# Optimization experiments

Measured on AMD Instinct MI355X. Metric: run time of the kernel, lower is better.

## Reference

```python
import jax, jax.numpy as jnp
import numpy as np

SCALE = 0.0078125  # dequant scale from init_kwargs


def setup_inputs() -> dict:
    key = jax.random.key(0)
    k1, k2, k3 = jax.random.split(key, 3)
    B, S, D_IN, D_OUT = 4, 2048, 2048, 8192
    x = jax.random.normal(k1, (B, S, D_IN), dtype=jnp.float32)
    weight = jax.random.normal(k2, (D_OUT, D_IN), dtype=jnp.float32)  # torch Linear layout
    bias = jax.random.normal(k3, (D_OUT,), dtype=jnp.float32)
    return {"x": x, "weight": weight, "bias": bias}


def reference(x, weight, bias):
    # MATMUL.apply(x, weight.t(), bias, scale): scaled matmul + fused bias
    # out[b,s,o] = scale * sum_i x[b,s,i] * weight[o,i] + bias[o]
    out = jnp.einsum('bsi,oi->bso', x, weight) * jnp.asarray(SCALE, x.dtype)
    return out + bias
```

## Files before the change

kernel.cpp:

```cpp
#include <hip/hip_runtime.h>
#include <hip/hip_bf16.h>
#include <stdint.h>

typedef __bf16 bf16x8 __attribute__((ext_vector_type(8)));
typedef float  f32x4  __attribute__((ext_vector_type(4)));
typedef float  f32x16 __attribute__((ext_vector_type(16)));

static constexpr float kScale = 0.0078125f;

static __device__ __forceinline__ uint32_t bf16_rne(float f) {
  uint32_t u = __builtin_bit_cast(uint32_t, f);
  u += 0x7FFFu + ((u >> 16) & 1u);
  return u >> 16;
}
static __device__ __forceinline__ uint32_t pack2(float lo, float hi) {
  return bf16_rne(lo) | (bf16_rne(hi) << 16);
}

__global__ __launch_bounds__(256) void cvt_fused(
    const float* __restrict__ x, const float* __restrict__ w,
    uint4* __restrict__ dst, long nx8 ) {
  const long i = (long)blockIdx.x * 256 + threadIdx.x;
  const float4* sv;
  long j;
  if (i < nx8) { sv = reinterpret_cast<const float4*>(x); j = i; }
  else         { sv = reinterpret_cast<const float4*>(w); j = i - nx8; }
  float4 a = sv[2 * j];
  float4 b = sv[2 * j + 1];
  uint4 o;
  o.x = pack2(a.x, a.y);
  o.y = pack2(a.z, a.w);
  o.z = pack2(b.x, b.y);
  o.w = pack2(b.z, b.w);
  dst[i] = o;
}

__global__ __launch_bounds__(256) void cvt_f32_to_bf16(
    const float* __restrict__ src, uint4* __restrict__ dst) {
  const int i = blockIdx.x * 256 + threadIdx.x;
  const float4* sv = reinterpret_cast<const float4*>(src);
  float4 a = sv[2 * i];
  float4 b = sv[2 * i + 1];
  uint4 o;
  o.x = pack2(a.x, a.y);
  o.y = pack2(a.z, a.w);
  o.z = pack2(b.x, b.y);
  o.w = pack2(b.z, b.w);
  dst[i] = o;
}

static __device__ __forceinline__ void gload_lds16(const void* g, void* l) {
  __builtin_amdgcn_global_load_lds(
      (const __attribute__((address_space(1))) void*)g,
      (__attribute__((address_space(3))) void*)l, 16, 0, 0);
}

#define BARRIER() __builtin_amdgcn_s_barrier()
#define VMW(n) asm volatile("s_waitcnt vmcnt(" #n ")" ::: "memory")

constexpr int TILE_V = (256 * 64) / 8;

template <int MH, int NH>
__device__ __forceinline__ void quad32(f32x16 (&acc)[4][2],
                                       const bf16x8 (&aF)[2][4],
                                       const bf16x8 (&bF)[4]) {
  __builtin_amdgcn_s_setprio(1);
#pragma unroll
  for (int ks = 0; ks < 4; ++ks)
#pragma unroll
    for (int mt = 0; mt < 2; ++mt)
      acc[MH * 2 + mt][NH] = __builtin_amdgcn_mfma_f32_32x32x16_bf16(
          aF[mt][ks], bF[ks], acc[MH * 2 + mt][NH], 0, 0, 0);
  __builtin_amdgcn_s_setprio(0);
}

template <int BUF, int MH>
__device__ __forceinline__ void loadA32(bf16x8 (&aF)[2][4], const bf16x8* Av,
                                        int wr, int l31, int erk) {
#pragma unroll
  for (int ks = 0; ks < 4; ++ks)
#pragma unroll
    for (int mt = 0; mt < 2; ++mt) {
      const int row = (MH << 7) + (wr << 6) + (mt << 5) + l31;
      aF[mt][ks] = Av[BUF * TILE_V + row * 8 + ((ks << 1) ^ erk)];
    }
}
template <int BUF, int NH>
__device__ __forceinline__ void loadB32(bf16x8 (&bF)[4], const bf16x8* Bv,
                                        int wc, int l31, int erk) {
  const int row = (NH << 7) + (wc << 5) + l31;
#pragma unroll
  for (int ks = 0; ks < 4; ++ks)
    bF[ks] = Bv[BUF * TILE_V + row * 8 + ((ks << 1) ^ erk)];
}

__global__ __launch_bounds__(512, 2) void gemm256_8phase(
    const uint16_t* __restrict__ A, const uint16_t* __restrict__ B,
    const float* __restrict__ bias, float* __restrict__ C,
    int Mi, int Ni, int Ki) {
  __shared__ __align__(16) uint16_t As[2][256 * 64];
  __shared__ __align__(16) uint16_t Bs[2][256 * 64];

  const int tid = threadIdx.x;
  const int l   = tid & 63;
  const int wv  = tid >> 6;
  const int wr  = wv >> 2;
  const int wc  = wv & 3;
  const int l31 = l & 31;
  const int lk  = l >> 5;
  const int l8  = l >> 3;
  const int l7  = l & 7;

  const int erk = l7 ^ ((l31 >> 3) & 3) ^ lk ^ (lk << 2);

  const int nbm = Mi >> 8, nbn = Ni >> 8;
  const int nwg = nbm * nbn;
  const int q = nwg >> 3, r = nwg & 7;
  const int xcd = (int)blockIdx.x & 7, orig = (int)blockIdx.x >> 3;
  const int swz = (xcd < r ? xcd * (q + 1) : r * (q + 1) + (xcd - r) * q) + orig;

  int bm, bn;
  if ((nbm & 7) == 0 && (nbn & 3) == 0) {
    const int s = swz >> 5;
    const int o = swz & 31;
    const int nsc = nbn >> 2;
    bm = (s / nsc) * 8 + (o >> 2);
    bn = (s % nsc) * 4 + (o & 3);
  } else {
    bm = swz / nbn;
    bn = swz % nbn;
  }

  const int u0   = l7 ^ l8 ^ (wv & 3);
  const int xcol = (u0 ^ ((u0 & 1) << 2)) << 3;
  const uint16_t* gA0 = A + (size_t)((bm << 8) + (wv << 3) + l8) * Ki + xcol;
  const uint16_t* gB0 = B + (size_t)((bn << 8) + (wv << 3) + l8) * Ki + xcol;

#define STAGE_A(bufi, chunk, t)                        \
  gload_lds16(gA0 + (size_t)(chunk) * Ki + (t) * 64,   \
              &As[bufi][((chunk) + (wv << 3)) << 6])
#define STAGE_B(bufi, chunk, t)                        \
  gload_lds16(gB0 + (size_t)(chunk) * Ki + (t) * 64,   \
              &Bs[bufi][((chunk) + (wv << 3)) << 6])

  const bf16x8* Av = reinterpret_cast<const bf16x8*>(&As[0][0]);
  const bf16x8* Bv = reinterpret_cast<const bf16x8*>(&Bs[0][0]);

  f32x16 acc[4][2] = {};
  bf16x8 aF[2][4], b0[4], b1[4];

  const int NT = Ki >> 6;
  const int NI = NT >> 1;

  STAGE_A(0, 0, 0);   STAGE_A(0, 64, 0);
  STAGE_B(0, 0, 0);   STAGE_B(0, 64, 0);
  STAGE_B(0, 128, 0); STAGE_B(0, 192, 0);
  STAGE_A(0, 128, 0); STAGE_A(0, 192, 0);
  STAGE_A(1, 0, 1);   STAGE_A(1, 64, 1);
  STAGE_B(1, 0, 1);   STAGE_B(1, 64, 1);
  STAGE_B(1, 128, 1); STAGE_B(1, 192, 1);
  VMW(6);
  BARRIER();

#pragma unroll 1
  for (int i = 0; i < NI - 1; ++i) {
    const int t1 = 2 * i + 1, t2 = 2 * i + 2, t3 = 2 * i + 3;

    loadB32<0, 0>(b0, Bv, wc, l31, erk);
    loadA32<0, 0>(aF, Av, wr, l31, erk);
    STAGE_A(1, 128, t1); STAGE_A(1, 192, t1);
    quad32<0, 0>(acc, aF, b0);
    BARRIER();

    loadB32<0, 1>(b1, Bv, wc, l31, erk);
    STAGE_A(0, 0, t2); STAGE_A(0, 64, t2);
    quad32<0, 1>(acc, aF, b1);
    BARRIER();

    loadA32<0, 1>(aF, Av, wr, l31, erk);
    STAGE_B(0, 0, t2); STAGE_B(0, 64, t2);
    quad32<1, 0>(acc, aF, b0);
    BARRIER();

    STAGE_B(0, 128, t2); STAGE_B(0, 192, t2);
    quad32<1, 1>(acc, aF, b1);
    VMW(6);
    BARRIER();

    loadB32<1, 0>(b0, Bv, wc, l31, erk);
    loadA32<1, 0>(aF, Av, wr, l31, erk);
    STAGE_A(0, 128, t2); STAGE_A(0, 192, t2);
    quad32<0, 0>(acc, aF, b0);
    BARRIER();

    loadB32<1, 1>(b1, Bv, wc, l31, erk);
    STAGE_A(1, 0, t3); STAGE_A(1, 64, t3);
    quad32<0, 1>(acc, aF, b1);
    BARRIER();

    loadA32<1, 1>(aF, Av, wr, l31, erk);
    STAGE_B(1, 0, t3); STAGE_B(1, 64, t3);
    quad32<1, 0>(acc, aF, b0);
    BARRIER();

    STAGE_B(1, 128, t3); STAGE_B(1, 192, t3);
    quad32<1, 1>(acc, aF, b1);
    VMW(6);
    BARRIER();
  }

  {
    const int t1 = NT - 1;
    loadB32<0, 0>(b0, Bv, wc, l31, erk);
    loadA32<0, 0>(aF, Av, wr, l31, erk);
    STAGE_A(1, 128, t1); STAGE_A(1, 192, t1);
    quad32<0, 0>(acc, aF, b0);
    BARRIER();
    loadB32<0, 1>(b1, Bv, wc, l31, erk);
    quad32<0, 1>(acc, aF, b1);
    BARRIER();
    loadA32<0, 1>(aF, Av, wr, l31, erk);
    quad32<1, 0>(acc, aF, b0);
    BARRIER();
    quad32<1, 1>(acc, aF, b1);
    VMW(0);
    BARRIER();
    loadB32<1, 0>(b0, Bv, wc, l31, erk);
    loadA32<1, 0>(aF, Av, wr, l31, erk);
    quad32<0, 0>(acc, aF, b0);
    BARRIER();
    loadB32<1, 1>(b1, Bv, wc, l31, erk);
    quad32<0, 1>(acc, aF, b1);
    BARRIER();
    loadA32<1, 1>(aF, Av, wr, l31, erk);
    quad32<1, 0>(acc, aF, b0);
    BARRIER();
    quad32<1, 1>(acc, aF, b1);
  }

  const int rowB = (bm << 8) + (wr << 6) + 4 * lk;
  const int colB = (bn << 8) + (wc << 5) + l31;
#pragma unroll
  for (int mt4 = 0; mt4 < 4; ++mt4) {
    const int rBase = rowB + (mt4 >> 1) * 128 + (mt4 & 1) * 32;
#pragma unroll
    for (int nh = 0; nh < 2; ++nh) {
      const int col = colB + nh * 128;
      const float bv = bias[col];
#pragma unroll
      for (int reg = 0; reg < 16; ++reg) {
        const int row = rBase + (reg & 3) + 8 * (reg >> 2);
        C[(size_t)row * Ni + col] = acc[mt4][nh][reg] * kScale + bv;
      }
    }
  }
}

__global__ __launch_bounds__(256) void gemm_bf16_bias(
    const uint16_t* __restrict__ A, const uint16_t* __restrict__ B,
    const float* __restrict__ bias, float* __restrict__ C,
    int Mi, int Ni, int Ki) {
  __shared__ __align__(16) uint16_t As[128 * 32];
  __shared__ __align__(16) uint16_t Bs[128 * 32];

  const int tid  = threadIdx.x;
  const int lane = tid & 63;
  const int wv   = tid >> 6;
  const int wr   = wv >> 1;
  const int wc   = wv & 1;
  const int fr   = lane & 15;
  const int fh   = lane >> 4;

  const int nTilesN = Ni >> 7;
  const int nwg = gridDim.x;
  const int q = nwg >> 3, r = nwg & 7;
  const int xcd = (int)blockIdx.x & 7, orig = (int)blockIdx.x >> 3;
  const int swz = (xcd < r ? xcd * (q + 1) : r * (q + 1) + (xcd - r) * q) + orig;
  const int bm = swz / nTilesN;
  const int bn = swz % nTilesN;

  const int sRow = tid >> 2;
  const int sCol = (tid & 3) << 3;

  const uint16_t* gA0 = A + (size_t)(bm * 128 + sRow) * Ki + sCol;
  const uint16_t* gA1 = gA0 + (size_t)64 * Ki;
  const uint16_t* gB0 = B + (size_t)(bn * 128 + sRow) * Ki + sCol;
  const uint16_t* gB1 = gB0 + (size_t)64 * Ki;
  uint16_t* lA0 = &As[tid * 8];
  uint16_t* lA1 = &As[(256 + tid) * 8];
  uint16_t* lB0 = &Bs[tid * 8];
  uint16_t* lB1 = &Bs[(256 + tid) * 8];

  const bf16x8* Av = reinterpret_cast<const bf16x8*>(As);
  const bf16x8* Bv = reinterpret_cast<const bf16x8*>(Bs);

  f32x4 acc[4][4] = {};

  for (int k0 = 0; k0 < Ki; k0 += 32) {
    gload_lds16(gA0 + k0, lA0);
    gload_lds16(gA1 + k0, lA1);
    gload_lds16(gB0 + k0, lB0);
    gload_lds16(gB1 + k0, lB1);
    __syncthreads();

    bf16x8 af[4], bfr[4];
#pragma unroll
    for (int m = 0; m < 4; ++m) af[m] = Av[(wr * 64 + m * 16 + fr) * 4 + fh];
#pragma unroll
    for (int n = 0; n < 4; ++n) bfr[n] = Bv[(wc * 64 + n * 16 + fr) * 4 + fh];

#pragma unroll
    for (int m = 0; m < 4; ++m)
#pragma unroll
      for (int n = 0; n < 4; ++n)
        acc[m][n] = __builtin_amdgcn_mfma_f32_16x16x32_bf16(af[m], bfr[n],
                                                            acc[m][n], 0, 0, 0);
    __syncthreads();
  }

  const int rowBase = bm * 128 + wr * 64;
  const int colBase = bn * 128 + wc * 64;
#pragma unroll
  for (int n = 0; n < 4; ++n) {
    const int col = colBase + n * 16 + fr;
    const float bv = bias[col];
#pragma unroll
    for (int m = 0; m < 4; ++m) {
      const int row = rowBase + m * 16 + fh * 4;
#pragma unroll
      for (int j = 0; j < 4; ++j)
        C[(size_t)(row + j) * Ni + col] = acc[m][n][j] * kScale + bv;
    }
  }
}

__global__ void naive_gemm(const float* __restrict__ x, const float* __restrict__ w,
                           const float* __restrict__ bias, float* __restrict__ out,
                           int Mi, int Ni, int Ki) {
  long idx = (long)blockIdx.x * blockDim.x + threadIdx.x;
  if (idx >= (long)Mi * Ni) return;
  int m = (int)(idx / Ni), n = (int)(idx % Ni);
  float s = 0.f;
  for (int k = 0; k < Ki; ++k) s += x[(long)m * Ki + k] * w[(long)n * Ki + k];
  out[idx] = s * kScale + bias[n];
}

extern "C" void kernel_launch(void* const* d_in, const int* in_sizes, int n_in,
                              void* d_out, int out_size, void* d_ws, size_t ws_size,
                              hipStream_t stream) {
  const float* x    = (const float*)d_in[0];
  const float* w    = (const float*)d_in[1];
  const float* bias = (const float*)d_in[2];
  float* out = (float*)d_out;

  const int Ni = in_sizes[2];
  const int Ki = in_sizes[1] / Ni;
  const int Mi = in_sizes[0] / Ki;

  const size_t nx = (size_t)Mi * Ki;
  const size_t nw = (size_t)Ni * Ki;

  if (ws_size >= (nx + nw) * sizeof(uint16_t) && (Ki % 32) == 0 &&
      (Mi % 128) == 0 && (Ni % 128) == 0) {
    uint16_t* xb = (uint16_t*)d_ws;
    uint16_t* wb = xb + nx;

    if ((nx % 2048) == 0 && (nw % 2048) == 0) {
      long total8 = (long)((nx + nw) / 8);
      cvt_fused<<<(int)(total8 / 256), 256, 0, stream>>>(x, w, (uint4*)xb,
                                                         (long)(nx / 8));
    } else {
      cvt_f32_to_bf16<<<(int)(nx / 2048), 256, 0, stream>>>(x, (uint4*)xb);
      cvt_f32_to_bf16<<<(int)(nw / 2048), 256, 0, stream>>>(w, (uint4*)wb);
    }

    if ((Mi % 256) == 0 && (Ni % 256) == 0 && (Ki % 128) == 0 && Ki >= 256) {
      dim3 grid((Mi / 256) * (Ni / 256));
      gemm256_8phase<<<grid, 512, 0, stream>>>(xb, wb, bias, out, Mi, Ni, Ki);
    } else {
      dim3 grid((Mi / 128) * (Ni / 128));
      gemm_bf16_bias<<<grid, 256, 0, stream>>>(xb, wb, bias, out, Mi, Ni, Ki);
    }
  } else {
    long total = (long)Mi * Ni;
    naive_gemm<<<(int)((total + 255) / 256), 256, 0, stream>>>(x, w, bias, out,
                                                               Mi, Ni, Ki);
  }
}
```

Baseline: 322.3 us.

## Replace 256x256 8-phase GEMM with 128x128 tile 2-phase pipelined kernel

Swaps the 512-thread 256x256-tile GEMM for a 256-thread 128x128-tile kernel, with each wave computing a 64x64 subtile and the K loop reduced to two phases per tile. The grid is four times larger and per-block LDS is cut to a quarter, which allows more resident blocks and fewer barriers per K step. The cost is lower arithmetic intensity per tile and more global and L2 traffic for A and B.

```diff
diff --git a/kernel.cpp b/kernel.cpp
--- a/kernel.cpp
+++ b/kernel.cpp
@@ -19,7 +19,7 @@
 
 __global__ __launch_bounds__(256) void cvt_fused(
     const float* __restrict__ x, const float* __restrict__ w,
-    uint4* __restrict__ dst, long nx8 ) {
+    uint4* __restrict__ dst, long nx8) {
   const long i = (long)blockIdx.x * 256 + threadIdx.x;
   const float4* sv;
   long j;
@@ -58,62 +58,61 @@
 #define BARRIER() __builtin_amdgcn_s_barrier()
 #define VMW(n) asm volatile("s_waitcnt vmcnt(" #n ")" ::: "memory")
 
-constexpr int TILE_V = (256 * 64) / 8;
-
-template <int MH, int NH>
-__device__ __forceinline__ void quad32(f32x16 (&acc)[4][2],
-                                       const bf16x8 (&aF)[2][4],
-                                       const bf16x8 (&bF)[4]) {
+constexpr int TV128 = (128 * 64) / 8;
+
+template <int MT>
+__device__ __forceinline__ void quad2(f32x16 (&acc)[2][2],
+                                      const bf16x8 (&aF)[4],
+                                      const bf16x8 (&bF)[2][4]) {
   __builtin_amdgcn_s_setprio(1);
 #pragma unroll
   for (int ks = 0; ks < 4; ++ks)
 #pragma unroll
-    for (int mt = 0; mt < 2; ++mt)
-      acc[MH * 2 + mt][NH] = __builtin_amdgcn_mfma_f32_32x32x16_bf16(
-          aF[mt][ks], bF[ks], acc[MH * 2 + mt][NH], 0, 0, 0);
+    for (int nt = 0; nt < 2; ++nt)
+      acc[MT][nt] = __builtin_amdgcn_mfma_f32_32x32x16_bf16(
+          aF[ks], bF[nt][ks], acc[MT][nt], 0, 0, 0);
   __builtin_amdgcn_s_setprio(0);
 }
 
-template <int BUF, int MH>
-__device__ __forceinline__ void loadA32(bf16x8 (&aF)[2][4], const bf16x8* Av,
+template <int BUF, int MT>
+__device__ __forceinline__ void loadAmt(bf16x8 (&aF)[4], const bf16x8* Av,
                                         int wr, int l31, int erk) {
+  const int row = (wr << 6) + (MT << 5) + l31;
 #pragma unroll
   for (int ks = 0; ks < 4; ++ks)
-#pragma unroll
-    for (int mt = 0; mt < 2; ++mt) {
-      const int row = (MH << 7) + (wr << 6) + (mt << 5) + l31;
-      aF[mt][ks] = Av[BUF * TILE_V + row * 8 + ((ks << 1) ^ erk)];
-    }
-}
-template <int BUF, int NH>
-__device__ __forceinline__ void loadB32(bf16x8 (&bF)[4], const bf16x8* Bv,
-                                        int wc, int l31, int erk) {
-  const int row = (NH << 7) + (wc << 5) + l31;
-#pragma unroll
-  for (int ks = 0; ks < 4; ++ks)
-    bF[ks] = Bv[BUF * TILE_V + row * 8 + ((ks << 1) ^ erk)];
-}
-
-__global__ __launch_bounds__(512, 2) void gemm256_8phase(
+    aF[ks] = Av[BUF * TV128 + row * 8 + ((ks << 1) ^ erk)];
+}
+template <int BUF>
+__device__ __forceinline__ void loadBall(bf16x8 (&bF)[2][4], const bf16x8* Bv,
+                                         int wc, int l31, int erk) {
+#pragma unroll
+  for (int nt = 0; nt < 2; ++nt) {
+    const int row = (wc << 6) + (nt << 5) + l31;
+#pragma unroll
+    for (int ks = 0; ks < 4; ++ks)
+      bF[nt][ks] = Bv[BUF * TV128 + row * 8 + ((ks << 1) ^ erk)];
+  }
+}
+
+__global__ __launch_bounds__(256, 2) void gemm128_2ph(
     const uint16_t* __restrict__ A, const uint16_t* __restrict__ B,
     const float* __restrict__ bias, float* __restrict__ C,
     int Mi, int Ni, int Ki) {
-  __shared__ __align__(16) uint16_t As[2][256 * 64];
-  __shared__ __align__(16) uint16_t Bs[2][256 * 64];
+  __shared__ __align__(16) uint16_t As[2][128 * 64];
+  __shared__ __align__(16) uint16_t Bs[2][128 * 64];
 
   const int tid = threadIdx.x;
   const int l   = tid & 63;
   const int wv  = tid >> 6;
-  const int wr  = wv >> 2;
-  const int wc  = wv & 3;
+  const int wr  = wv >> 1;
+  const int wc  = wv & 1;
   const int l31 = l & 31;
   const int lk  = l >> 5;
   const int l8  = l >> 3;
   const int l7  = l & 7;
-
   const int erk = l7 ^ ((l31 >> 3) & 3) ^ lk ^ (lk << 2);
 
-  const int nbm = Mi >> 8, nbn = Ni >> 8;
+  const int nbm = Mi >> 7, nbn = Ni >> 7;
   const int nwg = nbm * nbn;
   const int q = nwg >> 3, r = nwg & 7;
   const int xcd = (int)blockIdx.x & 7, orig = (int)blockIdx.x >> 3;
@@ -131,34 +130,32 @@
     bn = swz % nbn;
   }
 
-  const int u0   = l7 ^ l8 ^ (wv & 3);
+  const int u0   = l7 ^ l8 ^ wv;
   const int xcol = (u0 ^ ((u0 & 1) << 2)) << 3;
-  const uint16_t* gA0 = A + (size_t)((bm << 8) + (wv << 3) + l8) * Ki + xcol;
-  const uint16_t* gB0 = B + (size_t)((bn << 8) + (wv << 3) + l8) * Ki + xcol;
-
-#define STAGE_A(bufi, chunk, t)                        \
+  const uint16_t* gA0 = A + (size_t)((bm << 7) + (wv << 3) + l8) * Ki + xcol;
+  const uint16_t* gB0 = B + (size_t)((bn << 7) + (wv << 3) + l8) * Ki + xcol;
+
+#define STG_A(bufi, chunk, t)                          \
   gload_lds16(gA0 + (size_t)(chunk) * Ki + (t) * 64,   \
-              &As[bufi][((chunk) + (wv << 3)) << 6])
-#define STAGE_B(bufi, chunk, t)                        \
+              &As[bufi][((chunk) << 6) + (wv << 9)])
+#define STG_B(bufi, chunk, t)                          \
   gload_lds16(gB0 + (size_t)(chunk) * Ki + (t) * 64,   \
-              &Bs[bufi][((chunk) + (wv << 3)) << 6])
+              &Bs[bufi][((chunk) << 6) + (wv << 9)])
 
   const bf16x8* Av = reinterpret_cast<const bf16x8*>(&As[0][0]);
   const bf16x8* Bv = reinterpret_cast<const bf16x8*>(&Bs[0][0]);
 
-  f32x16 acc[4][2] = {};
-  bf16x8 aF[2][4], b0[4], b1[4];
+  f32x16 acc[2][2] = {};
+  bf16x8 aF[4], bF[2][4];
 
   const int NT = Ki >> 6;
   const int NI = NT >> 1;
 
-  STAGE_A(0, 0, 0);   STAGE_A(0, 64, 0);
-  STAGE_B(0, 0, 0);   STAGE_B(0, 64, 0);
-  STAGE_B(0, 128, 0); STAGE_B(0, 192, 0);
-  STAGE_A(0, 128, 0); STAGE_A(0, 192, 0);
-  STAGE_A(1, 0, 1);   STAGE_A(1, 64, 1);
-  STAGE_B(1, 0, 1);   STAGE_B(1, 64, 1);
-  STAGE_B(1, 128, 1); STAGE_B(1, 192, 1);
+  STG_A(0, 0, 0);  STG_A(0, 64, 0);
+  STG_A(0, 32, 0); STG_A(0, 96, 0);
+  STG_B(0, 0, 0);  STG_B(0, 32, 0);  STG_B(0, 64, 0);  STG_B(0, 96, 0);
+  STG_A(1, 0, 1);  STG_A(1, 64, 1);
+  STG_B(1, 0, 1);  STG_B(1, 32, 1);  STG_B(1, 64, 1);  STG_B(1, 96, 1);
   VMW(6);
   BARRIER();
 
@@ -166,91 +163,65 @@
   for (int i = 0; i < NI - 1; ++i) {
     const int t1 = 2 * i + 1, t2 = 2 * i + 2, t3 = 2 * i + 3;
 
-    loadB32<0, 0>(b0, Bv, wc, l31, erk);
-    loadA32<0, 0>(aF, Av, wr, l31, erk);
-    STAGE_A(1, 128, t1); STAGE_A(1, 192, t1);
-    quad32<0, 0>(acc, aF, b0);
-    BARRIER();
-
-    loadB32<0, 1>(b1, Bv, wc, l31, erk);
-    STAGE_A(0, 0, t2); STAGE_A(0, 64, t2);
-    quad32<0, 1>(acc, aF, b1);
-    BARRIER();
-
-    loadA32<0, 1>(aF, Av, wr, l31, erk);
-    STAGE_B(0, 0, t2); STAGE_B(0, 64, t2);
-    quad32<1, 0>(acc, aF, b0);
-    BARRIER();
-
-    STAGE_B(0, 128, t2); STAGE_B(0, 192, t2);
-    quad32<1, 1>(acc, aF, b1);
+    loadBall<0>(bF, Bv, wc, l31, erk);
+    loadAmt<0, 0>(aF, Av, wr, l31, erk);
+    STG_A(1, 32, t1); STG_A(1, 96, t1);
+    quad2<0>(acc, aF, bF);
+    BARRIER();
+
+    loadAmt<0, 1>(aF, Av, wr, l31, erk);
+    STG_A(0, 0, t2); STG_A(0, 64, t2);
+    STG_B(0, 0, t2); STG_B(0, 32, t2); STG_B(0, 64, t2); STG_B(0, 96, t2);
+    quad2<1>(acc, aF, bF);
     VMW(6);
     BARRIER();
 
-    loadB32<1, 0>(b0, Bv, wc, l31, erk);
-    loadA32<1, 0>(aF, Av, wr, l31, erk);
-    STAGE_A(0, 128, t2); STAGE_A(0, 192, t2);
-    quad32<0, 0>(acc, aF, b0);
-    BARRIER();
-
-    loadB32<1, 1>(b1, Bv, wc, l31, erk);
-    STAGE_A(1, 0, t3); STAGE_A(1, 64, t3);
-    quad32<0, 1>(acc, aF, b1);
-    BARRIER();
-
-    loadA32<1, 1>(aF, Av, wr, l31, erk);
-    STAGE_B(1, 0, t3); STAGE_B(1, 64, t3);
-    quad32<1, 0>(acc, aF, b0);
-    BARRIER();
-
-    STAGE_B(1, 128, t3); STAGE_B(1, 192, t3);
-    quad32<1, 1>(acc, aF, b1);
+    loadBall<1>(bF, Bv, wc, l31, erk);
+    loadAmt<1, 0>(aF, Av, wr, l31, erk);
+    STG_A(0, 32, t2); STG_A(0, 96, t2);
+    quad2<0>(acc, aF, bF);
+    BARRIER();
+
+    loadAmt<1, 1>(aF, Av, wr, l31, erk);
+    STG_A(1, 0, t3); STG_A(1, 64, t3);
+    STG_B(1, 0, t3); STG_B(1, 32, t3); STG_B(1, 64, t3); STG_B(1, 96, t3);
+    quad2<1>(acc, aF, bF);
     VMW(6);
     BARRIER();
   }
 
   {
     const int t1 = NT - 1;
-    loadB32<0, 0>(b0, Bv, wc, l31, erk);
-    loadA32<0, 0>(aF, Av, wr, l31, erk);
-    STAGE_A(1, 128, t1); STAGE_A(1, 192, t1);
-    quad32<0, 0>(acc, aF, b0);
-    BARRIER();
-    loadB32<0, 1>(b1, Bv, wc, l31, erk);
-    quad32<0, 1>(acc, aF, b1);
-    BARRIER();
-    loadA32<0, 1>(aF, Av, wr, l31, erk);
-    quad32<1, 0>(acc, aF, b0);
-    BARRIER();
-    quad32<1, 1>(acc, aF, b1);
+    loadBall<0>(bF, Bv, wc, l31, erk);
+    loadAmt<0, 0>(aF, Av, wr, l31, erk);
+    STG_A(1, 32, t1); STG_A(1, 96, t1);
+    quad2<0>(acc, aF, bF);
+    BARRIER();
+    loadAmt<0, 1>(aF, Av, wr, l31, erk);
+    quad2<1>(acc, aF, bF);
     VMW(0);
     BARRIER();
-    loadB32<1, 0>(b0, Bv, wc, l31, erk);
-    loadA32<1, 0>(aF, Av, wr, l31, erk);
-    quad32<0, 0>(acc, aF, b0);
-    BARRIER();
-    loadB32<1, 1>(b1, Bv, wc, l31, erk);
-    quad32<0, 1>(acc, aF, b1);
-    BARRIER();
-    loadA32<1, 1>(aF, Av, wr, l31, erk);
-    quad32<1, 0>(acc, aF, b0);
-    BARRIER();
-    quad32<1, 1>(acc, aF, b1);
-  }
-
-  const int rowB = (bm << 8) + (wr << 6) + 4 * lk;
-  const int colB = (bn << 8) + (wc << 5) + l31;
-#pragma unroll
-  for (int mt4 = 0; mt4 < 4; ++mt4) {
-    const int rBase = rowB + (mt4 >> 1) * 128 + (mt4 & 1) * 32;
-#pragma unroll
-    for (int nh = 0; nh < 2; ++nh) {
-      const int col = colB + nh * 128;
+    loadBall<1>(bF, Bv, wc, l31, erk);
+    loadAmt<1, 0>(aF, Av, wr, l31, erk);
+    quad2<0>(acc, aF, bF);
+    BARRIER();
+    loadAmt<1, 1>(aF, Av, wr, l31, erk);
+    quad2<1>(acc, aF, bF);
+  }
+
+  const int rowB = (bm << 7) + (wr << 6) + 4 * lk;
+  const int colB = (bn << 7) + (wc << 6) + l31;
+#pragma unroll
+  for (int mt = 0; mt < 2; ++mt) {
+    const int rBase = rowB + mt * 32;
+#pragma unroll
+    for (int nt = 0; nt < 2; ++nt) {
+      const int col = colB + nt * 32;
       const float bv = bias[col];
 #pragma unroll
       for (int reg = 0; reg < 16; ++reg) {
         const int row = rBase + (reg & 3) + 8 * (reg >> 2);
-        C[(size_t)row * Ni + col] = acc[mt4][nh][reg] * kScale + bv;
+        C[(size_t)row * Ni + col] = acc[mt][nt][reg] * kScale + bv;
       }
     }
   }
@@ -374,9 +345,9 @@
       cvt_f32_to_bf16<<<(int)(nw / 2048), 256, 0, stream>>>(w, (uint4*)wb);
     }
 
-    if ((Mi % 256) == 0 && (Ni % 256) == 0 && (Ki % 128) == 0 && Ki >= 256) {
-      dim3 grid((Mi / 256) * (Ni / 256));
-      gemm256_8phase<<<grid, 512, 0, stream>>>(xb, wb, bias, out, Mi, Ni, Ki);
+    if ((Ki % 128) == 0 && Ki >= 256) {
+      dim3 grid((Mi / 128) * (Ni / 128));
+      gemm128_2ph<<<grid, 256, 0, stream>>>(xb, wb, bias, out, Mi, Ni, Ki);
     } else {
       dim3 grid((Mi / 128) * (Ni / 128));
       gemm_bf16_bias<<<grid, 256, 0, stream>>>(xb, wb, bias, out, Mi, Ni, Ki);
```

After: 340.9 us. 1.06x slower.
